# Performance work log

Hardware: AMD Instinct MI355X
Metric: run time of the kernel (lower is better)

Reference implementation:

```python
import jax, jax.numpy as jnp
import numpy as np

B, T_IN, T_OUT, F, H = 1024, 168, 24, 8, 256


def _lstm_step(x, h, c, Wih, Whh, bih, bhh):
    # x: [B, in], h/c: [B, H]; PyTorch gate order i, f, g, o
    g = x @ Wih.T + h @ Whh.T + bih + bhh
    i, f, gg, o = jnp.split(g, 4, axis=-1)
    i = jax.nn.sigmoid(i)
    f = jax.nn.sigmoid(f)
    gg = jnp.tanh(gg)
    o = jax.nn.sigmoid(o)
    c2 = f * c + i * gg
    h2 = o * jnp.tanh(c2)
    return h2, c2


def _run_lstm(xs, Wih, Whh, bih, bhh):
    # xs: [T, B, in] -> (ys [T,B,H], h_T, c_T)
    Bs = xs.shape[1]
    h0 = jnp.zeros((Bs, H), xs.dtype)
    c0 = jnp.zeros((Bs, H), xs.dtype)
    def step(carry, x):
        h, c = carry
        h2, c2 = _lstm_step(x, h, c, Wih, Whh, bih, bhh)
        return (h2, c2), h2
    (hT, cT), ys = jax.lax.scan(step, (h0, c0), xs)
    return ys, hT, cT


def _forward(x, enc_Wih0, enc_Whh0, enc_bih0, enc_bhh0,
             enc_Wih1, enc_Whh1, enc_bih1, enc_bhh1,
             dec_Wih, dec_Whh, dec_bih, dec_bhh,
             fc1_W, fc1_b, attn_in_W, attn_in_b,
             attn_out_W, attn_out_b, fc2_W, fc2_b):
    scale = 1.0 / jnp.sqrt(jnp.asarray(H, x.dtype))

    # ---- encoder: 2-layer LSTM ----
    xs = jnp.transpose(x, (1, 0, 2))  # [T, B, F]
    ys0, h0, c0 = _run_lstm(xs, enc_Wih0, enc_Whh0, enc_bih0, enc_bhh0)
    _, h1, c1 = _run_lstm(ys0, enc_Wih1, enc_Whh1, enc_bih1, enc_bhh1)
    h_mean = (h0 + h1) * 0.5  # mean over layers, [B, H]
    c_mean = (c0 + c1) * 0.5

    # per-decoder initial state (same mean state for every decoder at t=0)
    h_state = jnp.tile(h_mean[None], (F, 1, 1))  # [F, B, H]
    c_state = jnp.tile(c_mean[None], (F, 1, 1))
    dec_in = x[:, -1, :]  # [B, F]

    def dec_one(xi, h, c, Wih, Whh, bih, bhh, f1W, f1b, inW, inb, oW, ob, f2W, f2b):
        # xi: [B, 1], single-feature single-step LSTM decode
        h2, c2 = _lstm_step(xi, h, c, Wih, Whh, bih, bhh)  # [B, H]
        a = jax.nn.leaky_relu(h2 @ f1W.T + f1b, 0.01)  # q = k = v
        qkv = a @ inW.T + inb  # [B, 3H]
        q, k, v = jnp.split(qkv, 3, axis=-1)
        # NB: faithful to the original bug: MultiheadAttention sees the batch
        # dim as the sequence dim, so attention is over the B examples.
        attn = jax.nn.softmax((q @ k.T) * scale, axis=-1)  # [B, B]
        ao = (attn @ v) @ oW.T + ob  # [B, H]
        out = jax.nn.leaky_relu(ao @ f2W.T + f2b, 0.01)  # [B, 1]
        return out[:, 0], h2, c2

    dec_all = jax.vmap(dec_one)  # over the F decoders

    def outer(carry, _):
        h, c, din = carry
        xi = din.T[:, :, None]  # [F, B, 1]
        out, h2, c2 = dec_all(xi, h, c, dec_Wih, dec_Whh, dec_bih, dec_bhh,
                              fc1_W, fc1_b, attn_in_W, attn_in_b,
                              attn_out_W, attn_out_b, fc2_W, fc2_b)
        return (h2, c2, out.T), out  # out: [F, B]

    _, outs = jax.lax.scan(outer, (h_state, c_state, dec_in), None, length=T_OUT)
    return jnp.transpose(outs, (2, 0, 1))  # [B, T_OUT, F]


def setup_inputs() -> dict:
    key = jax.random.key(0)
    ks = jax.random.split(key, 22)
    p = lambda k, shape: jax.random.normal(k, shape, dtype=jnp.float32) * 0.05
    return {
        "x": jax.random.normal(ks[0], (B, T_IN, F), dtype=jnp.float32),
        "enc_Wih0": p(ks[1], (4 * H, F)),
        "enc_Whh0": p(ks[2], (4 * H, H)),
        "enc_bih0": p(ks[3], (4 * H,)),
        "enc_bhh0": p(ks[4], (4 * H,)),
        "enc_Wih1": p(ks[5], (4 * H, H)),
        "enc_Whh1": p(ks[6], (4 * H, H)),
        "enc_bih1": p(ks[7], (4 * H,)),
        "enc_bhh1": p(ks[8], (4 * H,)),
        "dec_Wih": p(ks[9], (F, 4 * H, 1)),
        "dec_Whh": p(ks[10], (F, 4 * H, H)),
        "dec_bih": p(ks[11], (F, 4 * H)),
        "dec_bhh": p(ks[12], (F, 4 * H)),
        "fc1_W": p(ks[13], (F, H, H)),
        "fc1_b": p(ks[14], (F, H)),
        "attn_in_W": p(ks[15], (F, 3 * H, H)),
        "attn_in_b": p(ks[16], (F, 3 * H)),
        "attn_out_W": p(ks[17], (F, H, H)),
        "attn_out_b": p(ks[18], (F, H)),
        "fc2_W": p(ks[19], (F, 1, H)),
        "fc2_b": p(ks[20], (F, 1)),
    }


def reference(x, enc_Wih0, enc_Whh0, enc_bih0, enc_bhh0,
              enc_Wih1, enc_Whh1, enc_bih1, enc_bhh1,
              dec_Wih, dec_Whh, dec_bih, dec_bhh,
              fc1_W, fc1_b, attn_in_W, attn_in_b,
              attn_out_W, attn_out_b, fc2_W, fc2_b):
    return _forward(x, enc_Wih0, enc_Whh0, enc_bih0, enc_bhh0,
                    enc_Wih1, enc_Whh1, enc_bih1, enc_bhh1,
                    dec_Wih, dec_Whh, dec_bih, dec_bhh,
                    fc1_W, fc1_b, attn_in_W, attn_in_b,
                    attn_out_W, attn_out_b, fc2_W, fc2_b)
```

## Files before the change

### kernel.cpp

```cpp
#include <hip/hip_runtime.h>
#include <math.h>

#define H 256
#define H4 1024
#define Bsz 1024
#define TIN 168
#define TOUT 24
#define Fh 8
#define XROW (TIN*Fh)
#define BH ((size_t)Bsz * H)
#define SL32 ((size_t)Bsz * 32)

typedef __attribute__((ext_vector_type(8))) short bf16x8;
typedef __attribute__((ext_vector_type(4))) float f32x4;

__device__ __forceinline__ ushort f2bf(float f) {
    union { float f; unsigned u; } v; v.f = f;
    unsigned r = v.u + 0x7fff + ((v.u >> 16) & 1);
    return (ushort)(r >> 16);
}
__device__ __forceinline__ float bf2f(ushort u) {
    union { unsigned u; float f; } v; v.u = ((unsigned)u) << 16;
    return v.f;
}
__device__ __forceinline__ float sigmf(float x) {
    return __fdividef(1.0f, 1.0f + __expf(-x));
}
__device__ __forceinline__ float tanhf_(float x) {
    const float e = __expf(-2.0f * fabsf(x));
    const float t = __fdividef(1.0f - e, 1.0f + e);
    return copysignf(t, x);
}

__device__ __forceinline__ void load_coh4(const ushort* p0, const ushort* p1,
                                          const ushort* p2, const ushort* p3,
                                          f32x4& a, f32x4& b, f32x4& c, f32x4& d)
{
    asm volatile(
        "global_load_dwordx4 %0, %4, off sc0 sc1\n\t"
        "global_load_dwordx4 %1, %5, off sc0 sc1\n\t"
        "global_load_dwordx4 %2, %6, off sc0 sc1\n\t"
        "global_load_dwordx4 %3, %7, off sc0 sc1\n\t"
        "s_waitcnt vmcnt(0)"
        : "=&v"(a), "=&v"(b), "=&v"(c), "=&v"(d)
        : "v"(p0), "v"(p1), "v"(p2), "v"(p3)
        : "memory");
}
__device__ __forceinline__ void load_coh8(const ushort* p0, const ushort* p1,
                                          const ushort* p2, const ushort* p3,
                                          const ushort* p4, const ushort* p5,
                                          const ushort* p6, const ushort* p7,
                                          f32x4& a, f32x4& b, f32x4& c, f32x4& d,
                                          f32x4& e, f32x4& f, f32x4& g, f32x4& h)
{
    asm volatile(
        "global_load_dwordx4 %0, %8, off sc0 sc1\n\t"
        "global_load_dwordx4 %1, %9, off sc0 sc1\n\t"
        "global_load_dwordx4 %2, %10, off sc0 sc1\n\t"
        "global_load_dwordx4 %3, %11, off sc0 sc1\n\t"
        "global_load_dwordx4 %4, %12, off sc0 sc1\n\t"
        "global_load_dwordx4 %5, %13, off sc0 sc1\n\t"
        "global_load_dwordx4 %6, %14, off sc0 sc1\n\t"
        "global_load_dwordx4 %7, %15, off sc0 sc1\n\t"
        "s_waitcnt vmcnt(0)"
        : "=&v"(a), "=&v"(b), "=&v"(c), "=&v"(d),
          "=&v"(e), "=&v"(f), "=&v"(g), "=&v"(h)
        : "v"(p0), "v"(p1), "v"(p2), "v"(p3), "v"(p4), "v"(p5), "v"(p6), "v"(p7)
        : "memory");
}
__device__ __forceinline__ void load_coh4f(const float* p0, const float* p1,
                                           const float* p2, const float* p3,
                                           float& a, float& b, float& c, float& d)
{
    asm volatile(
        "global_load_dword %0, %4, off sc0 sc1\n\t"
        "global_load_dword %1, %5, off sc0 sc1\n\t"
        "global_load_dword %2, %6, off sc0 sc1\n\t"
        "global_load_dword %3, %7, off sc0 sc1\n\t"
        "s_waitcnt vmcnt(0)"
        : "=&v"(a), "=&v"(b), "=&v"(c), "=&v"(d)
        : "v"(p0), "v"(p1), "v"(p2), "v"(p3)
        : "memory");
}
__device__ __forceinline__ void store_coh8B(ushort* p, uint2 v) {
    asm volatile("global_store_dwordx2 %0, %1, off sc0 sc1"
                 :: "v"(p), "v"(v) : "memory");
}
__device__ __forceinline__ void store_coh16B(float* p, f32x4 v) {
    asm volatile("global_store_dwordx4 %0, %1, off sc0 sc1"
                 :: "v"(p), "v"(v) : "memory");
}

__device__ __forceinline__ void load_l2_8(const ushort* p0, const ushort* p1,
                                          const ushort* p2, const ushort* p3,
                                          const ushort* p4, const ushort* p5,
                                          const ushort* p6, const ushort* p7,
                                          f32x4& a, f32x4& b, f32x4& c, f32x4& d,
                                          f32x4& e, f32x4& f, f32x4& g, f32x4& h)
{
    asm volatile(
        "global_load_dwordx4 %0, %8, off sc0\n\t"
        "global_load_dwordx4 %1, %9, off sc0\n\t"
        "global_load_dwordx4 %2, %10, off sc0\n\t"
        "global_load_dwordx4 %3, %11, off sc0\n\t"
        "global_load_dwordx4 %4, %12, off sc0\n\t"
        "global_load_dwordx4 %5, %13, off sc0\n\t"
        "global_load_dwordx4 %6, %14, off sc0\n\t"
        "global_load_dwordx4 %7, %15, off sc0\n\t"
        "s_waitcnt vmcnt(0)"
        : "=&v"(a), "=&v"(b), "=&v"(c), "=&v"(d),
          "=&v"(e), "=&v"(f), "=&v"(g), "=&v"(h)
        : "v"(p0), "v"(p1), "v"(p2), "v"(p3), "v"(p4), "v"(p5), "v"(p6), "v"(p7)
        : "memory");
}
__device__ __forceinline__ void load_l2_f4(const float* p, f32x4& v) {
    asm volatile(
        "global_load_dwordx4 %0, %1, off sc0\n\t"
        "s_waitcnt vmcnt(0)"
        : "=&v"(v) : "v"(p) : "memory");
}

__device__ __forceinline__ void gbar(unsigned* cnt, unsigned target) {
    asm volatile("s_waitcnt vmcnt(0)" ::: "memory");
    __syncthreads();
    if (threadIdx.x == 0) {
        __hip_atomic_fetch_add(cnt, 1u, __ATOMIC_RELAXED, __HIP_MEMORY_SCOPE_AGENT);
        int sp = 0;
        while (__hip_atomic_fetch_add(cnt, 0u, __ATOMIC_RELAXED,
                                      __HIP_MEMORY_SCOPE_AGENT) < target) {
            __builtin_amdgcn_s_sleep(2);
            if (++sp > 20000) break;
        }
    }
    __syncthreads();
    asm volatile("" ::: "memory");
}

__global__ __launch_bounds__(256)
void cast_f32_bf16(const float* __restrict__ in, ushort* __restrict__ out, int n) {
    int i = blockIdx.x * 256 + threadIdx.x;
    const int stride = gridDim.x * 256;
    for (; i < n; i += stride) out[i] = f2bf(in[i]);
// ... 27 lines not shown
    u[f * 256 + tid] = su;
    if (tid == 0) {
        float dd = 0.f, cc = 0.f;
        for (int n = 0; n < 256; ++n) dd += wsh[n] * inb[f * 768 + 512 + n];
        for (int i = 0; i < 256; ++i) cc += ob[f * 256 + i] * f2W[f * 256 + i];
        dconst[f] = dd;
        ccv[f] = cc + f2b[f];
    }
}

struct MP {
    const float *x, *ebih0, *ebhh0, *ebih1, *ebhh1;
    const ushort *Whh0, *Wih0p, *Wih1, *Whh1;
    ushort *h0A, *h0B, *h1A, *h1B, *hm;
    float *cm;
    const ushort *dWhh, *f1Wb, *inWb;
    const float *dWih, *dbih, *dbhh, *f1b, *inb, *u, *dconst, *ccv;
    ushort *kb0, *kb1;
    float *vw0, *vw1, *out;
    unsigned *bar;
};

__global__ __launch_bounds__(256, 1)
void mega2(MP P)
{
    __shared__ ushort SA[32][264];
    __shared__ ushort SB[32][264];
    __shared__ ushort SC[32][264];
    __shared__ float pre[4][32][36];
    __shared__ ushort xL[32][32];
    __shared__ ushort h2s[32][264];
    __shared__ ushort as2[32][264];
    __shared__ ushort qs[32][264];
    __shared__ float tri[4][2][16][3];
    __shared__ float dinL[32];

    const int bid = blockIdx.x;
    const int tid = threadIdx.x;
    const int l = tid & 63, w = tid >> 6;
    const int lr = l & 15, lq = l >> 4, lk = lq * 8;

    {
        const int grp = bid >> 3, wgi = bid & 7;
        const int rowbase = grp * 32;
        const int ub = wgi * 32;
        unsigned* cnt = P.bar + grp * 32;
        const int g = w;
        const int sS = tid >> 5, sR = tid & 31;

        for (int e = tid; e < 32 * 32; e += 256) (&xL[0][0])[e] = 0;

        const int crow = tid >> 3;
        const int cu = (tid & 7) * 4;
        float c0v[4] = {0,0,0,0}, c1v[4] = {0,0,0,0};
        float h0v[4] = {0,0,0,0}, h1v[4] = {0,0,0,0};

        float b0s[2], b1s[2];
#pragma unroll
        for (int n = 0; n < 2; ++n) {
            const int j = ub + n * 16 + lr;
            b0s[n] = P.ebih0[g * H + j] + P.ebhh0[g * H + j];
            b1s[n] = P.ebih1[g * H + j] + P.ebhh1[g * H + j];
        }
        unsigned bph = 0;
        __syncthreads();

        for (int t = 0; t < TIN; ++t) {
            const int p = t & 1;
            const ushort* h0r = p ? P.h0B : P.h0A;
            ushort*       h0w = p ? P.h0A : P.h0B;
            const ushort* h1r = p ? P.h1B : P.h1A;
            ushort*       h1w = p ? P.h1A : P.h1B;

            {
                const ushort* s0 = h0r + sS * SL32 + (size_t)(rowbase + sR) * 32;
                f32x4 v0, v1, v2, v3;
                load_coh4(s0, s0 + 8, s0 + 16, s0 + 24, v0, v1, v2, v3);
                *(f32x4*)&SA[sR][sS * 32 + 0]  = v0;
                *(f32x4*)&SA[sR][sS * 32 + 8]  = v1;
                *(f32x4*)&SA[sR][sS * 32 + 16] = v2;
                *(f32x4*)&SA[sR][sS * 32 + 24] = v3;
                xL[tid >> 3][tid & 7] =
                    f2bf(P.x[(size_t)(rowbase + (tid >> 3)) * XROW + t * Fh + (tid & 7)]);
            }
            __syncthreads();
            {
                bf16x8 am[2][8], ax[2];
#pragma unroll
                for (int m = 0; m < 2; ++m) {
#pragma unroll
                    for (int k = 0; k < 8; ++k)
                        am[m][k] = *(const bf16x8*)&SA[m * 16 + lr][k * 32 + lk];
                    ax[m] = *(const bf16x8*)&xL[m * 16 + lr][lk];
                }
                f32x4 acc[2][2] = {};
#pragma unroll
                for (int n = 0; n < 2; ++n) {
                    const ushort* wp = P.Whh0 + (size_t)(g * H + ub + n * 16 + lr) * H + lk;
#pragma unroll
                    for (int k = 0; k < 8; ++k) {
                        const bf16x8 b8 = *(const bf16x8*)(wp + k * 32);
                        acc[0][n] = __builtin_amdgcn_mfma_f32_16x16x32_bf16(am[0][k], b8, acc[0][n], 0, 0, 0);
                        acc[1][n] = __builtin_amdgcn_mfma_f32_16x16x32_bf16(am[1][k], b8, acc[1][n], 0, 0, 0);
                    }
                    const bf16x8 bx = *(const bf16x8*)(P.Wih0p + (size_t)(g * H + ub + n * 16 + lr) * 32 + lk);
                    acc[0][n] = __builtin_amdgcn_mfma_f32_16x16x32_bf16(ax[0], bx, acc[0][n], 0, 0, 0);
                    acc[1][n] = __builtin_amdgcn_mfma_f32_16x16x32_bf16(ax[1], bx, acc[1][n], 0, 0, 0);
                }
#pragma unroll
                for (int m = 0; m < 2; ++m)
#pragma unroll
                    for (int n = 0; n < 2; ++n)
#pragma unroll
                        for (int r = 0; r < 4; ++r)
                            pre[g][m * 16 + lq * 4 + r][n * 16 + lr] = acc[m][n][r] + b0s[n];
            }
            __syncthreads();
            {
                const f32x4 pi = *(const f32x4*)&pre[0][crow][cu];
                const f32x4 pf = *(const f32x4*)&pre[1][crow][cu];
                const f32x4 pg = *(const f32x4*)&pre[2][crow][cu];
                const f32x4 po = *(const f32x4*)&pre[3][crow][cu];
#pragma unroll
                for (int j = 0; j < 4; ++j) {
                    const float ig = sigmf(pi[j]);
                    const float fg = sigmf(pf[j]);
                    const float gg = tanhf_(pg[j]);
                    const float og = sigmf(po[j]);
                    c0v[j] = fg * c0v[j] + ig * gg;
                    h0v[j] = og * tanhf_(c0v[j]);
                }
                uint2 hp;
                hp.x = (unsigned)f2bf(h0v[0]) | ((unsigned)f2bf(h0v[1]) << 16);
                hp.y = (unsigned)f2bf(h0v[2]) | ((unsigned)f2bf(h0v[3]) << 16);
                store_coh8B(h0w + wgi * SL32 + (size_t)(rowbase + crow) * 32 + cu, hp);
            }
            gbar(cnt, ++bph * 8u);
            {
                const ushort* s0 = h0w + sS * SL32 + (size_t)(rowbase + sR) * 32;
                const ushort* s1 = h1r + sS * SL32 + (size_t)(rowbase + sR) * 32;
                f32x4 a0, a1, a2, a3, b0, b1, b2, b3;
                load_coh8(s0, s0 + 8, s0 + 16, s0 + 24,
                          s1, s1 + 8, s1 + 16, s1 + 24,
                          a0, a1, a2, a3, b0, b1, b2, b3);
                *(f32x4*)&SB[sR][sS * 32 + 0]  = a0;
                *(f32x4*)&SB[sR][sS * 32 + 8]  = a1;
                *(f32x4*)&SB[sR][sS * 32 + 16] = a2;
                *(f32x4*)&SB[sR][sS * 32 + 24] = a3;
                *(f32x4*)&SC[sR][sS * 32 + 0]  = b0;
                *(f32x4*)&SC[sR][sS * 32 + 8]  = b1;
                *(f32x4*)&SC[sR][sS * 32 + 16] = b2;
                *(f32x4*)&SC[sR][sS * 32 + 24] = b3;
            }
            __syncthreads();
            {
                bf16x8 an[2][8], ah[2][8];
#pragma unroll
                for (int m = 0; m < 2; ++m)
#pragma unroll
                    for (int k = 0; k < 8; ++k) {
                        an[m][k] = *(const bf16x8*)&SB[m * 16 + lr][k * 32 + lk];
                        ah[m][k] = *(const bf16x8*)&SC[m * 16 + lr][k * 32 + lk];
                    }
                f32x4 acc[2][2] = {};
#pragma unroll
                for (int n = 0; n < 2; ++n) {
                    const ushort* w1 = P.Wih1 + (size_t)(g * H + ub + n * 16 + lr) * H + lk;
                    const ushort* w2 = P.Whh1 + (size_t)(g * H + ub + n * 16 + lr) * H + lk;
#pragma unroll
                    for (int k = 0; k < 8; ++k) {
                        const bf16x8 b1 = *(const bf16x8*)(w1 + k * 32);
                        acc[0][n] = __builtin_amdgcn_mfma_f32_16x16x32_bf16(an[0][k], b1, acc[0][n], 0, 0, 0);
                        acc[1][n] = __builtin_amdgcn_mfma_f32_16x16x32_bf16(an[1][k], b1, acc[1][n], 0, 0, 0);
                        const bf16x8 b2 = *(const bf16x8*)(w2 + k * 32);
                        acc[0][n] = __builtin_amdgcn_mfma_f32_16x16x32_bf16(ah[0][k], b2, acc[0][n], 0, 0, 0);
                        acc[1][n] = __builtin_amdgcn_mfma_f32_16x16x32_bf16(ah[1][k], b2, acc[1][n], 0, 0, 0);
                    }
                }
#pragma unroll
                for (int m = 0; m < 2; ++m)
#pragma unroll
                    for (int n = 0; n < 2; ++n)
#pragma unroll
                        for (int r = 0; r < 4; ++r)
                            pre[g][m * 16 + lq * 4 + r][n * 16 + lr] = acc[m][n][r] + b1s[n];
            }
            __syncthreads();
            {
                const f32x4 pi = *(const f32x4*)&pre[0][crow][cu];
                const f32x4 pf = *(const f32x4*)&pre[1][crow][cu];
                const f32x4 pg = *(const f32x4*)&pre[2][crow][cu];
                const f32x4 po = *(const f32x4*)&pre[3][crow][cu];
#pragma unroll
                for (int j = 0; j < 4; ++j) {
                    const float ig = sigmf(pi[j]);
                    const float fg = sigmf(pf[j]);
                    const float gg = tanhf_(pg[j]);
                    const float og = sigmf(po[j]);
                    c1v[j] = fg * c1v[j] + ig * gg;
                    h1v[j] = og * tanhf_(c1v[j]);
                }
                uint2 hp;
                hp.x = (unsigned)f2bf(h1v[0]) | ((unsigned)f2bf(h1v[1]) << 16);
                hp.y = (unsigned)f2bf(h1v[2]) | ((unsigned)f2bf(h1v[3]) << 16);
                store_coh8B(h1w + wgi * SL32 + (size_t)(rowbase + crow) * 32 + cu, hp);
            }
            gbar(cnt, ++bph * 8u);
        }
        {
            uint2 hp;
            hp.x = (unsigned)f2bf(0.5f * (h0v[0] + h1v[0]))
                 | ((unsigned)f2bf(0.5f * (h0v[1] + h1v[1])) << 16);
            hp.y = (unsigned)f2bf(0.5f * (h0v[2] + h1v[2]))
                 | ((unsigned)f2bf(0.5f * (h0v[3] + h1v[3])) << 16);
            store_coh8B(P.hm + (size_t)(rowbase + crow) * 256 + ub + cu, hp);
            f32x4 cv;
#pragma unroll
            for (int j = 0; j < 4; ++j) cv[j] = 0.5f * (c0v[j] + c1v[j]);
            store_coh16B(P.cm + (size_t)(rowbase + crow) * 256 + ub + cu, cv);
        }
    }
    gbar(P.bar + 2048, 256u);

    {
        const int f = bid & 7, mb = bid >> 3;
        const int m0 = mb * 32;

#pragma unroll
        for (int it = 0; it < 4; ++it) {
            const int idx = tid + it * 256;
            const int r = idx >> 5, c16 = (idx & 31) * 8;
            f32x4 v0, v1, v2, v3;
            const ushort* pbase = P.hm + (size_t)(m0 + r) * 256 + c16;
            asm volatile("global_load_dwordx4 %0, %1, off sc0 sc1\n\ts_waitcnt vmcnt(0)"
                         : "=&v"(v0) : "v"(pbase) : "memory");
            *(f32x4*)&h2s[r][c16] = v0;
            (void)v1; (void)v2; (void)v3;
        }
        float cd[2][4][4];
#pragma unroll
        for (int m = 0; m < 2; ++m)
#pragma unroll
            for (int jt = 0; jt < 4; ++jt) {
                const float* pc = P.cm + (size_t)(m0 + m * 16 + lq * 4) * 256
                                + (w * 64 + jt * 16 + lr);
                load_coh4f(pc, pc + 256, pc + 512, pc + 768,
                           cd[m][jt][0], cd[m][jt][1], cd[m][jt][2], cd[m][jt][3]);
            }
        float bsum[4][4], wxr[4][4];
#pragma unroll
        for (int jt = 0; jt < 4; ++jt)
#pragma unroll
            for (int g = 0; g < 4; ++g) {
                const int j = w * 64 + jt * 16 + lr;
                bsum[jt][g] = P.dbih[f * H4 + g * H + j] + P.dbhh[f * H4 + g * H + j];
                wxr[jt][g] = P.dWih[f * H4 + g * H + j];
            }
        __syncthreads();

        unsigned* fcnt = P.bar + 1024 + f * 32;
// ... 114 lines not shown
#pragma unroll 1
                for (int rr = 0; rr < 8; ++rr) {
                    const int mloc = w * 8 + rr;
                    const ushort4 a4 = *(const ushort4*)&as2[mloc][l * 4];
                    float s = bf2f(a4.x) * u4.x + bf2f(a4.y) * u4.y
                            + bf2f(a4.z) * u4.z + bf2f(a4.w) * u4.w;
#pragma unroll
                    for (int d = 1; d < 64; d <<= 1) s += __shfl_xor(s, d);
                    if (l == 0) vwcur[f * Bsz + m0 + mloc] = s + P.dconst[f];
                }
            }
            gbar(fcnt, (unsigned)(t + 1) * 32u);
            {
                bf16x8 qf[2][8];
#pragma unroll
                for (int m = 0; m < 2; ++m)
#pragma unroll
                    for (int k = 0; k < 8; ++k)
                        qf[m][k] = *(const bf16x8*)&qs[m * 16 + lr][k * 32 + lk];
                float mM0 = -1e30f, lS0 = 0.f, oS0 = 0.f;
                float mM1 = -1e30f, lS1 = 0.f, oS1 = 0.f;
                const int kb0r = w * 256;
#pragma unroll 1
                for (int kf = 0; kf < 16; ++kf) {
                    const int kb = kb0r + kf * 16;
                    const ushort* base = kcur + ((size_t)f * Bsz + kb + lr) * H + lk;
                    f32x4 kr0, kr1, kr2, kr3, kr4, kr5, kr6, kr7;
                    load_l2_8(base, base + 32, base + 64, base + 96,
                              base + 128, base + 160, base + 192, base + 224,
                              kr0, kr1, kr2, kr3, kr4, kr5, kr6, kr7);
                    f32x4 acc0 = {}, acc1 = {};
                    {
                        const bf16x8 kk0 = *(bf16x8*)&kr0, kk1 = *(bf16x8*)&kr1,
                                     kk2 = *(bf16x8*)&kr2, kk3 = *(bf16x8*)&kr3,
                                     kk4 = *(bf16x8*)&kr4, kk5 = *(bf16x8*)&kr5,
                                     kk6 = *(bf16x8*)&kr6, kk7 = *(bf16x8*)&kr7;
                        acc0 = __builtin_amdgcn_mfma_f32_16x16x32_bf16(kk0, qf[0][0], acc0, 0, 0, 0);
                        acc1 = __builtin_amdgcn_mfma_f32_16x16x32_bf16(kk0, qf[1][0], acc1, 0, 0, 0);
                        acc0 = __builtin_amdgcn_mfma_f32_16x16x32_bf16(kk1, qf[0][1], acc0, 0, 0, 0);
                        acc1 = __builtin_amdgcn_mfma_f32_16x16x32_bf16(kk1, qf[1][1], acc1, 0, 0, 0);
                        acc0 = __builtin_amdgcn_mfma_f32_16x16x32_bf16(kk2, qf[0][2], acc0, 0, 0, 0);
                        acc1 = __builtin_amdgcn_mfma_f32_16x16x32_bf16(kk2, qf[1][2], acc1, 0, 0, 0);
                        acc0 = __builtin_amdgcn_mfma_f32_16x16x32_bf16(kk3, qf[0][3], acc0, 0, 0, 0);
                        acc1 = __builtin_amdgcn_mfma_f32_16x16x32_bf16(kk3, qf[1][3], acc1, 0, 0, 0);
                        acc0 = __builtin_amdgcn_mfma_f32_16x16x32_bf16(kk4, qf[0][4], acc0, 0, 0, 0);
                        acc1 = __builtin_amdgcn_mfma_f32_16x16x32_bf16(kk4, qf[1][4], acc1, 0, 0, 0);
                        acc0 = __builtin_amdgcn_mfma_f32_16x16x32_bf16(kk5, qf[0][5], acc0, 0, 0, 0);
                        acc1 = __builtin_amdgcn_mfma_f32_16x16x32_bf16(kk5, qf[1][5], acc1, 0, 0, 0);
                        acc0 = __builtin_amdgcn_mfma_f32_16x16x32_bf16(kk6, qf[0][6], acc0, 0, 0, 0);
                        acc1 = __builtin_amdgcn_mfma_f32_16x16x32_bf16(kk6, qf[1][6], acc1, 0, 0, 0);
                        acc0 = __builtin_amdgcn_mfma_f32_16x16x32_bf16(kk7, qf[0][7], acc0, 0, 0, 0);
                        acc1 = __builtin_amdgcn_mfma_f32_16x16x32_bf16(kk7, qf[1][7], acc1, 0, 0, 0);
                    }
                    f32x4 v4w;
                    load_l2_f4(vwcur + f * Bsz + kb + lq * 4, v4w);
                    {
                        const float mx = fmaxf(fmaxf(acc0[0], acc0[1]), fmaxf(acc0[2], acc0[3]));
                        const float mn = fmaxf(mM0, mx);
                        const float sc = __expf(mM0 - mn);
                        const float e0 = __expf(acc0[0] - mn), e1 = __expf(acc0[1] - mn);
                        const float e2 = __expf(acc0[2] - mn), e3 = __expf(acc0[3] - mn);
                        lS0 = lS0 * sc + (e0 + e1 + e2 + e3);
                        oS0 = oS0 * sc + (e0 * v4w[0] + e1 * v4w[1] + e2 * v4w[2] + e3 * v4w[3]);
                        mM0 = mn;
                    }
                    {
                        const float mx = fmaxf(fmaxf(acc1[0], acc1[1]), fmaxf(acc1[2], acc1[3]));
                        const float mn = fmaxf(mM1, mx);
                        const float sc = __expf(mM1 - mn);
                        const float e0 = __expf(acc1[0] - mn), e1 = __expf(acc1[1] - mn);
                        const float e2 = __expf(acc1[2] - mn), e3 = __expf(acc1[3] - mn);
                        lS1 = lS1 * sc + (e0 + e1 + e2 + e3);
                        oS1 = oS1 * sc + (e0 * v4w[0] + e1 * v4w[1] + e2 * v4w[2] + e3 * v4w[3]);
                        mM1 = mn;
                    }
                }
#pragma unroll
                for (int d = 16; d < 64; d <<= 1) {
                    {
                        const float m2 = __shfl_xor(mM0, d), l2 = __shfl_xor(lS0, d), o2 = __shfl_xor(oS0, d);
                        const float mn = fmaxf(mM0, m2);
                        const float sa = __expf(mM0 - mn), sb = __expf(m2 - mn);
                        lS0 = lS0 * sa + l2 * sb; oS0 = oS0 * sa + o2 * sb; mM0 = mn;
                    }
                    {
                        const float m2 = __shfl_xor(mM1, d), l2 = __shfl_xor(lS1, d), o2 = __shfl_xor(oS1, d);
                        const float mn = fmaxf(mM1, m2);
                        const float sa = __expf(mM1 - mn), sb = __expf(m2 - mn);
                        lS1 = lS1 * sa + l2 * sb; oS1 = oS1 * sa + o2 * sb; mM1 = mn;
                    }
                }
                if (l < 16) {
                    tri[w][0][l][0] = mM0; tri[w][0][l][1] = lS0; tri[w][0][l][2] = oS0;
                    tri[w][1][l][0] = mM1; tri[w][1][l][1] = lS1; tri[w][1][l][2] = oS1;
                }
                __syncthreads();
                if (tid < 32) {
// ... 51 lines not shown
    ushort* h1A = (ushort*)alloc(BH * 2);
    ushort* h0B = (ushort*)alloc(BH * 2);
    ushort* h1B = (ushort*)alloc(BH * 2);
    ushort* hm  = (ushort*)alloc(BH * 2);
    float*  cm  = (float*)alloc(BH * 4);
    ushort* kb0 = (ushort*)alloc(8 * BH * 2);
    ushort* kb1 = (ushort*)alloc(8 * BH * 2);
    float*  vw0 = (float*)alloc((size_t)Fh * Bsz * 4);
    float*  vw1 = (float*)alloc((size_t)Fh * Bsz * 4);
    float*  ubuf = (float*)alloc((size_t)Fh * H * 4);
    float*  dbuf = (float*)alloc(Fh * 4);
    float*  ccb  = (float*)alloc(Fh * 4);
    unsigned* bar = (unsigned*)alloc(3072 * 4);
    ushort* wWhh0 = (ushort*)alloc((size_t)H4 * H * 2);
    ushort* wWih0p= (ushort*)alloc((size_t)H4 * 32 * 2);
    ushort* wWih1 = (ushort*)alloc((size_t)H4 * H * 2);
    ushort* wWhh1 = (ushort*)alloc((size_t)H4 * H * 2);
    ushort* wdWhh = (ushort*)alloc((size_t)8 * H4 * H * 2);
    ushort* wf1W  = (ushort*)alloc((size_t)8 * H * H * 2);
    ushort* winW  = (ushort*)alloc((size_t)8 * 768 * H * 2);

    const dim3 blk(256);

    hipMemsetAsync(d_ws, 0, BH * 2 * 2, stream);
    hipMemsetAsync(bar, 0, 3072 * 4, stream);

    cast_f32_bf16<<<dim3(512), blk, 0, stream>>>(eWhh0, wWhh0, H4 * H);
    cast_f32_bf16<<<dim3(512), blk, 0, stream>>>(eWih1, wWih1, H4 * H);
    cast_f32_bf16<<<dim3(512), blk, 0, stream>>>(eWhh1, wWhh1, H4 * H);
    cast_pad_wih0<<<dim3(128), blk, 0, stream>>>(eWih0, wWih0p);
    cast_f32_bf16<<<dim3(1024), blk, 0, stream>>>(dWhh, wdWhh, 8 * H4 * H);
    cast_f32_bf16<<<dim3(512), blk, 0, stream>>>(f1W, wf1W, 8 * H * H);
    cast_f32_bf16<<<dim3(1024), blk, 0, stream>>>(inW, winW, 8 * 768 * H);
    precompute_kernel<<<dim3(8), blk, 0, stream>>>(oW, ob, f2W, f2b, inW, inb,
                                                   ubuf, dbuf, ccb);

    MP P;
    P.x = x; P.ebih0 = ebih0; P.ebhh0 = ebhh0; P.ebih1 = ebih1; P.ebhh1 = ebhh1;
    P.Whh0 = wWhh0; P.Wih0p = wWih0p; P.Wih1 = wWih1; P.Whh1 = wWhh1;
    P.h0A = h0A; P.h0B = h0B; P.h1A = h1A; P.h1B = h1B;
    P.hm = hm; P.cm = cm;
    P.dWhh = wdWhh; P.f1Wb = wf1W; P.inWb = winW;
    P.dWih = dWih; P.dbih = dbih; P.dbhh = dbhh; P.f1b = f1b; P.inb = inb;
    P.u = ubuf; P.dconst = dbuf; P.ccv = ccb;
    P.kb0 = kb0; P.kb1 = kb1; P.vw0 = vw0; P.vw1 = vw1;
    P.out = (float*)d_out; P.bar = bar;

    mega2<<<dim3(256), blk, 0, stream>>>(P);

    (void)in_sizes; (void)n_in; (void)out_size; (void)ws_size;
}
```

Measured before the change: 3.568 ms.

## Wavefront-pipeline encoder layers to halve grid barriers; batch attention key loads

The two-layer encoder loop is skewed so that layer 1 at step t-1 and layer 0 at step t run in the same iteration. Each step now needs one grid-wide barrier and one coherent load phase instead of two, and one shared h0 tile feeds both the layer-0 recurrent matmul and the layer-1 input matmul. The decoder attention loop is also unrolled by two: K and V loads for two 16-row chunks are issued together with immediate offsets before the waitcnt. The trade-off is one extra loop iteration, separate pre-activation buffers per layer, more registers, and a wider zero memset so both layers' h buffers start cleared.

Result: faster. 3.237 ms (-9.3%).

```diff
diff --git a/kernel.cpp b/kernel.cpp
--- a/kernel.cpp
+++ b/kernel.cpp
@@ -32,20 +32,6 @@
     return copysignf(t, x);
 }
 
-__device__ __forceinline__ void load_coh4(const ushort* p0, const ushort* p1,
-                                          const ushort* p2, const ushort* p3,
-                                          f32x4& a, f32x4& b, f32x4& c, f32x4& d)
-{
-    asm volatile(
-        "global_load_dwordx4 %0, %4, off sc0 sc1\n\t"
-        "global_load_dwordx4 %1, %5, off sc0 sc1\n\t"
-        "global_load_dwordx4 %2, %6, off sc0 sc1\n\t"
-        "global_load_dwordx4 %3, %7, off sc0 sc1\n\t"
-        "s_waitcnt vmcnt(0)"
-        : "=&v"(a), "=&v"(b), "=&v"(c), "=&v"(d)
-        : "v"(p0), "v"(p1), "v"(p2), "v"(p3)
-        : "memory");
-}
 __device__ __forceinline__ void load_coh8(const ushort* p0, const ushort* p1,
                                           const ushort* p2, const ushort* p3,
                                           const ushort* p4, const ushort* p5,
@@ -82,6 +68,10 @@
         : "v"(p0), "v"(p1), "v"(p2), "v"(p3)
         : "memory");
 }
+__device__ __forceinline__ void load_coh16Bx(const ushort* p, f32x4& v) {
+    asm volatile("global_load_dwordx4 %0, %1, off sc0 sc1\n\ts_waitcnt vmcnt(0)"
+                 : "=&v"(v) : "v"(p) : "memory");
+}
 __device__ __forceinline__ void store_coh8B(ushort* p, uint2 v) {
     asm volatile("global_store_dwordx2 %0, %1, off sc0 sc1"
                  :: "v"(p), "v"(v) : "memory");
@@ -89,35 +79,6 @@
 __device__ __forceinline__ void store_coh16B(float* p, f32x4 v) {
     asm volatile("global_store_dwordx4 %0, %1, off sc0 sc1"
                  :: "v"(p), "v"(v) : "memory");
-}
-
-__device__ __forceinline__ void load_l2_8(const ushort* p0, const ushort* p1,
-                                          const ushort* p2, const ushort* p3,
-                                          const ushort* p4, const ushort* p5,
-                                          const ushort* p6, const ushort* p7,
-                                          f32x4& a, f32x4& b, f32x4& c, f32x4& d,
-                                          f32x4& e, f32x4& f, f32x4& g, f32x4& h)
-{
-    asm volatile(
-        "global_load_dwordx4 %0, %8, off sc0\n\t"
-        "global_load_dwordx4 %1, %9, off sc0\n\t"
-        "global_load_dwordx4 %2, %10, off sc0\n\t"
-        "global_load_dwordx4 %3, %11, off sc0\n\t"
-        "global_load_dwordx4 %4, %12, off sc0\n\t"
-        "global_load_dwordx4 %5, %13, off sc0\n\t"
-        "global_load_dwordx4 %6, %14, off sc0\n\t"
-        "global_load_dwordx4 %7, %15, off sc0\n\t"
-        "s_waitcnt vmcnt(0)"
-        : "=&v"(a), "=&v"(b), "=&v"(c), "=&v"(d),
-          "=&v"(e), "=&v"(f), "=&v"(g), "=&v"(h)
-        : "v"(p0), "v"(p1), "v"(p2), "v"(p3), "v"(p4), "v"(p5), "v"(p6), "v"(p7)
-        : "memory");
-}
-__device__ __forceinline__ void load_l2_f4(const float* p, f32x4& v) {
-    asm volatile(
-        "global_load_dwordx4 %0, %1, off sc0\n\t"
-        "s_waitcnt vmcnt(0)"
-        : "=&v"(v) : "v"(p) : "memory");
 }
 
 __device__ __forceinline__ void gbar(unsigned* cnt, unsigned target) {
@@ -191,12 +152,12 @@
 };
 
 __global__ __launch_bounds__(256, 1)
-void mega2(MP P)
+void mega3(MP P)
 {
     __shared__ ushort SA[32][264];
-    __shared__ ushort SB[32][264];
     __shared__ ushort SC[32][264];
-    __shared__ float pre[4][32][36];
+    __shared__ float pre0[4][32][36];
+    __shared__ float pre1[4][32][36];
     __shared__ ushort xL[32][32];
     __shared__ ushort h2s[32][264];
     __shared__ ushort as2[32][264];
@@ -234,34 +195,45 @@
         unsigned bph = 0;
         __syncthreads();
 
-        for (int t = 0; t < TIN; ++t) {
-            const int p = t & 1;
-            const ushort* h0r = p ? P.h0B : P.h0A;
-            ushort*       h0w = p ? P.h0A : P.h0B;
-            const ushort* h1r = p ? P.h1B : P.h1A;
-            ushort*       h1w = p ? P.h1A : P.h1B;
+        for (int i = 0; i <= TIN; ++i) {
+            ushort*       h0wb = (i & 1) ? P.h0B : P.h0A;
+            const ushort* h0rb = (i & 1) ? P.h0A : P.h0B;
+            ushort*       h1wb = (i & 1) ? P.h1A : P.h1B;
+            const ushort* h1rb = (i & 1) ? P.h1B : P.h1A;
 
             {
-                const ushort* s0 = h0r + sS * SL32 + (size_t)(rowbase + sR) * 32;
-                f32x4 v0, v1, v2, v3;
-                load_coh4(s0, s0 + 8, s0 + 16, s0 + 24, v0, v1, v2, v3);
-                *(f32x4*)&SA[sR][sS * 32 + 0]  = v0;
-                *(f32x4*)&SA[sR][sS * 32 + 8]  = v1;
-                *(f32x4*)&SA[sR][sS * 32 + 16] = v2;
-                *(f32x4*)&SA[sR][sS * 32 + 24] = v3;
-                xL[tid >> 3][tid & 7] =
-                    f2bf(P.x[(size_t)(rowbase + (tid >> 3)) * XROW + t * Fh + (tid & 7)]);
+                const ushort* s0 = h0rb + sS * SL32 + (size_t)(rowbase + sR) * 32;
+                const ushort* s1 = h1rb + sS * SL32 + (size_t)(rowbase + sR) * 32;
+                f32x4 a0, a1, a2, a3, b0, b1, b2, b3;
+                load_coh8(s0, s0 + 8, s0 + 16, s0 + 24,
+                          s1, s1 + 8, s1 + 16, s1 + 24,
+                          a0, a1, a2, a3, b0, b1, b2, b3);
+                *(f32x4*)&SA[sR][sS * 32 + 0]  = a0;
+                *(f32x4*)&SA[sR][sS * 32 + 8]  = a1;
+                *(f32x4*)&SA[sR][sS * 32 + 16] = a2;
+                *(f32x4*)&SA[sR][sS * 32 + 24] = a3;
+                *(f32x4*)&SC[sR][sS * 32 + 0]  = b0;
+                *(f32x4*)&SC[sR][sS * 32 + 8]  = b1;
+                *(f32x4*)&SC[sR][sS * 32 + 16] = b2;
+                *(f32x4*)&SC[sR][sS * 32 + 24] = b3;
+                if (i < TIN)
+                    xL[tid >> 3][tid & 7] =
+                        f2bf(P.x[(size_t)(rowbase + (tid >> 3)) * XROW + i * Fh + (tid & 7)]);
             }
             __syncthreads();
-            {
-                bf16x8 am[2][8], ax[2];
-#pragma unroll
-                for (int m = 0; m < 2; ++m) {
-#pragma unroll
-                    for (int k = 0; k < 8; ++k)
-                        am[m][k] = *(const bf16x8*)&SA[m * 16 + lr][k * 32 + lk];
-                    ax[m] = *(const bf16x8*)&xL[m * 16 + lr][lk];
-                }
+
+            bf16x8 aS[2][8], aC[2][8], ax[2];
+#pragma unroll
+            for (int m = 0; m < 2; ++m) {
+#pragma unroll
+                for (int k = 0; k < 8; ++k) {
+                    aS[m][k] = *(const bf16x8*)&SA[m * 16 + lr][k * 32 + lk];
+                    aC[m][k] = *(const bf16x8*)&SC[m * 16 + lr][k * 32 + lk];
+                }
+                ax[m] = *(const bf16x8*)&xL[m * 16 + lr][lk];
+            }
+
+            if (i < TIN) {
                 f32x4 acc[2][2] = {};
 #pragma unroll
                 for (int n = 0; n < 2; ++n) {
@@ -269,8 +241,8 @@
 #pragma unroll
                     for (int k = 0; k < 8; ++k) {
                         const bf16x8 b8 = *(const bf16x8*)(wp + k * 32);
-                        acc[0][n] = __builtin_amdgcn_mfma_f32_16x16x32_bf16(am[0][k], b8, acc[0][n], 0, 0, 0);
-                        acc[1][n] = __builtin_amdgcn_mfma_f32_16x16x32_bf16(am[1][k], b8, acc[1][n], 0, 0, 0);
+                        acc[0][n] = __builtin_amdgcn_mfma_f32_16x16x32_bf16(aS[0][k], b8, acc[0][n], 0, 0, 0);
+                        acc[1][n] = __builtin_amdgcn_mfma_f32_16x16x32_bf16(aS[1][k], b8, acc[1][n], 0, 0, 0);
                     }
                     const bf16x8 bx = *(const bf16x8*)(P.Wih0p + (size_t)(g * H + ub + n * 16 + lr) * 32 + lk);
                     acc[0][n] = __builtin_amdgcn_mfma_f32_16x16x32_bf16(ax[0], bx, acc[0][n], 0, 0, 0);
@@ -282,14 +254,39 @@
                     for (int n = 0; n < 2; ++n)
 #pragma unroll
                         for (int r = 0; r < 4; ++r)
-                            pre[g][m * 16 + lq * 4 + r][n * 16 + lr] = acc[m][n][r] + b0s[n];
+                            pre0[g][m * 16 + lq * 4 + r][n * 16 + lr] = acc[m][n][r] + b0s[n];
+            }
+            if (i >= 1) {
+                f32x4 acc[2][2] = {};
+#pragma unroll
+                for (int n = 0; n < 2; ++n) {
+                    const ushort* w1 = P.Wih1 + (size_t)(g * H + ub + n * 16 + lr) * H + lk;
+                    const ushort* w2 = P.Whh1 + (size_t)(g * H + ub + n * 16 + lr) * H + lk;
+#pragma unroll
+                    for (int k = 0; k < 8; ++k) {
+                        const bf16x8 b1 = *(const bf16x8*)(w1 + k * 32);
+                        acc[0][n] = __builtin_amdgcn_mfma_f32_16x16x32_bf16(aS[0][k], b1, acc[0][n], 0, 0, 0);
+                        acc[1][n] = __builtin_amdgcn_mfma_f32_16x16x32_bf16(aS[1][k], b1, acc[1][n], 0, 0, 0);
+                        const bf16x8 b2 = *(const bf16x8*)(w2 + k * 32);
+                        acc[0][n] = __builtin_amdgcn_mfma_f32_16x16x32_bf16(aC[0][k], b2, acc[0][n], 0, 0, 0);
+                        acc[1][n] = __builtin_amdgcn_mfma_f32_16x16x32_bf16(aC[1][k], b2, acc[1][n], 0, 0, 0);
+                    }
+                }
+#pragma unroll
+                for (int m = 0; m < 2; ++m)
+#pragma unroll
+                    for (int n = 0; n < 2; ++n)
+#pragma unroll
+                        for (int r = 0; r < 4; ++r)
+                            pre1[g][m * 16 + lq * 4 + r][n * 16 + lr] = acc[m][n][r] + b1s[n];
             }
             __syncthreads();
-            {
-                const f32x4 pi = *(const f32x4*)&pre[0][crow][cu];
-                const f32x4 pf = *(const f32x4*)&pre[1][crow][cu];
-                const f32x4 pg = *(const f32x4*)&pre[2][crow][cu];
-                const f32x4 po = *(const f32x4*)&pre[3][crow][cu];
+
+            if (i < TIN) {
+                const f32x4 pi = *(const f32x4*)&pre0[0][crow][cu];
+                const f32x4 pf = *(const f32x4*)&pre0[1][crow][cu];
+                const f32x4 pg = *(const f32x4*)&pre0[2][crow][cu];
+                const f32x4 po = *(const f32x4*)&pre0[3][crow][cu];
 #pragma unroll
                 for (int j = 0; j < 4; ++j) {
                     const float ig = sigmf(pi[j]);
@@ -302,64 +299,13 @@
                 uint2 hp;
                 hp.x = (unsigned)f2bf(h0v[0]) | ((unsigned)f2bf(h0v[1]) << 16);
                 hp.y = (unsigned)f2bf(h0v[2]) | ((unsigned)f2bf(h0v[3]) << 16);
-                store_coh8B(h0w + wgi * SL32 + (size_t)(rowbase + crow) * 32 + cu, hp);
-            }
-            gbar(cnt, ++bph * 8u);
-            {
-                const ushort* s0 = h0w + sS * SL32 + (size_t)(rowbase + sR) * 32;
-                const ushort* s1 = h1r + sS * SL32 + (size_t)(rowbase + sR) * 32;
-                f32x4 a0, a1, a2, a3, b0, b1, b2, b3;
-                load_coh8(s0, s0 + 8, s0 + 16, s0 + 24,
-                          s1, s1 + 8, s1 + 16, s1 + 24,
-                          a0, a1, a2, a3, b0, b1, b2, b3);
-                *(f32x4*)&SB[sR][sS * 32 + 0]  = a0;
-                *(f32x4*)&SB[sR][sS * 32 + 8]  = a1;
-                *(f32x4*)&SB[sR][sS * 32 + 16] = a2;
-                *(f32x4*)&SB[sR][sS * 32 + 24] = a3;
-                *(f32x4*)&SC[sR][sS * 32 + 0]  = b0;
-                *(f32x4*)&SC[sR][sS * 32 + 8]  = b1;
-                *(f32x4*)&SC[sR][sS * 32 + 16] = b2;
-                *(f32x4*)&SC[sR][sS * 32 + 24] = b3;
-            }
-            __syncthreads();
-            {
-                bf16x8 an[2][8], ah[2][8];
-#pragma unroll
-                for (int m = 0; m < 2; ++m)
-#pragma unroll
-                    for (int k = 0; k < 8; ++k) {
-                        an[m][k] = *(const bf16x8*)&SB[m * 16 + lr][k * 32 + lk];
-                        ah[m][k] = *(const bf16x8*)&SC[m * 16 + lr][k * 32 + lk];
-                    }
-                f32x4 acc[2][2] = {};
-#pragma unroll
-                for (int n = 0; n < 2; ++n) {
-                    const ushort* w1 = P.Wih1 + (size_t)(g * H + ub + n * 16 + lr) * H + lk;
-                    const ushort* w2 = P.Whh1 + (size_t)(g * H + ub + n * 16 + lr) * H + lk;
-#pragma unroll
-                    for (int k = 0; k < 8; ++k) {
-                        const bf16x8 b1 = *(const bf16x8*)(w1 + k * 32);
-                        acc[0][n] = __builtin_amdgcn_mfma_f32_16x16x32_bf16(an[0][k], b1, acc[0][n], 0, 0, 0);
-                        acc[1][n] = __builtin_amdgcn_mfma_f32_16x16x32_bf16(an[1][k], b1, acc[1][n], 0, 0, 0);
-                        const bf16x8 b2 = *(const bf16x8*)(w2 + k * 32);
-                        acc[0][n] = __builtin_amdgcn_mfma_f32_16x16x32_bf16(ah[0][k], b2, acc[0][n], 0, 0, 0);
-                        acc[1][n] = __builtin_amdgcn_mfma_f32_16x16x32_bf16(ah[1][k], b2, acc[1][n], 0, 0, 0);
-                    }
-                }
-#pragma unroll
-                for (int m = 0; m < 2; ++m)
-#pragma unroll
-                    for (int n = 0; n < 2; ++n)
-#pragma unroll
-                        for (int r = 0; r < 4; ++r)
-                            pre[g][m * 16 + lq * 4 + r][n * 16 + lr] = acc[m][n][r] + b1s[n];
-            }
-            __syncthreads();
-            {
-                const f32x4 pi = *(const f32x4*)&pre[0][crow][cu];
-                const f32x4 pf = *(const f32x4*)&pre[1][crow][cu];
-                const f32x4 pg = *(const f32x4*)&pre[2][crow][cu];
-                const f32x4 po = *(const f32x4*)&pre[3][crow][cu];
+                store_coh8B(h0wb + wgi * SL32 + (size_t)(rowbase + crow) * 32 + cu, hp);
+            }
+            if (i >= 1) {
+                const f32x4 pi = *(const f32x4*)&pre1[0][crow][cu];
+                const f32x4 pf = *(const f32x4*)&pre1[1][crow][cu];
+                const f32x4 pg = *(const f32x4*)&pre1[2][crow][cu];
+                const f32x4 po = *(const f32x4*)&pre1[3][crow][cu];
 #pragma unroll
                 for (int j = 0; j < 4; ++j) {
                     const float ig = sigmf(pi[j]);
@@ -372,7 +318,7 @@
                 uint2 hp;
                 hp.x = (unsigned)f2bf(h1v[0]) | ((unsigned)f2bf(h1v[1]) << 16);
                 hp.y = (unsigned)f2bf(h1v[2]) | ((unsigned)f2bf(h1v[3]) << 16);
-                store_coh8B(h1w + wgi * SL32 + (size_t)(rowbase + crow) * 32 + cu, hp);
+                store_coh8B(h1wb + wgi * SL32 + (size_t)(rowbase + crow) * 32 + cu, hp);
             }
             gbar(cnt, ++bph * 8u);
         }
@@ -399,12 +345,9 @@
         for (int it = 0; it < 4; ++it) {
             const int idx = tid + it * 256;
             const int r = idx >> 5, c16 = (idx & 31) * 8;
-            f32x4 v0, v1, v2, v3;
-            const ushort* pbase = P.hm + (size_t)(m0 + r) * 256 + c16;
-            asm volatile("global_load_dwordx4 %0, %1, off sc0 sc1\n\ts_waitcnt vmcnt(0)"
-                         : "=&v"(v0) : "v"(pbase) : "memory");
+            f32x4 v0;
+            load_coh16Bx(P.hm + (size_t)(m0 + r) * 256 + c16, v0);
             *(f32x4*)&h2s[r][c16] = v0;
-            (void)v1; (void)v2; (void)v3;
         }
         float cd[2][4][4];
 #pragma unroll
@@ -565,57 +508,128 @@
                 float mM1 = -1e30f, lS1 = 0.f, oS1 = 0.f;
                 const int kb0r = w * 256;
 #pragma unroll 1
-                for (int kf = 0; kf < 16; ++kf) {
-                    const int kb = kb0r + kf * 16;
-                    const ushort* base = kcur + ((size_t)f * Bsz + kb + lr) * H + lk;
-                    f32x4 kr0, kr1, kr2, kr3, kr4, kr5, kr6, kr7;
-                    load_l2_8(base, base + 32, base + 64, base + 96,
-                              base + 128, base + 160, base + 192, base + 224,
-                              kr0, kr1, kr2, kr3, kr4, kr5, kr6, kr7);
-                    f32x4 acc0 = {}, acc1 = {};
+                for (int kf = 0; kf < 16; kf += 2) {
+                    const int kbA = kb0r + kf * 16;
+                    const ushort* baseA = kcur + ((size_t)f * Bsz + kbA + lr) * H + lk;
+                    const ushort* baseB = baseA + 16 * H;
+                    const float* pvA = vwcur + f * Bsz + kbA + lq * 4;
+                    const float* pvB = pvA + 16;
+                    f32x4 A0, A1, A2, A3, A4, A5, A6, A7;
+                    f32x4 B0, B1, B2, B3, B4, B5, B6, B7;
+                    f32x4 vA, vB;
+                    asm volatile(
+                        "global_load_dwordx4 %0, %18, off sc0\n\t"
+                        "global_load_dwordx4 %1, %18, off offset:64 sc0\n\t"
+                        "global_load_dwordx4 %2, %18, off offset:128 sc0\n\t"
+                        "global_load_dwordx4 %3, %18, off offset:192 sc0\n\t"
+                        "global_load_dwordx4 %4, %18, off offset:256 sc0\n\t"
+                        "global_load_dwordx4 %5, %18, off offset:320 sc0\n\t"
+                        "global_load_dwordx4 %6, %18, off offset:384 sc0\n\t"
+                        "global_load_dwordx4 %7, %18, off offset:448 sc0\n\t"
+                        "global_load_dwordx4 %8, %19, off sc0\n\t"
+                        "global_load_dwordx4 %9, %19, off offset:64 sc0\n\t"
+                        "global_load_dwordx4 %10, %19, off offset:128 sc0\n\t"
+                        "global_load_dwordx4 %11, %19, off offset:192 sc0\n\t"
+                        "global_load_dwordx4 %12, %19, off offset:256 sc0\n\t"
+                        "global_load_dwordx4 %13, %19, off offset:320 sc0\n\t"
+                        "global_load_dwordx4 %14, %19, off offset:384 sc0\n\t"
+                        "global_load_dwordx4 %15, %19, off offset:448 sc0\n\t"
+                        "global_load_dwordx4 %16, %20, off sc0\n\t"
+                        "global_load_dwordx4 %17, %21, off sc0\n\t"
+                        "s_waitcnt vmcnt(0)"
+                        : "=&v"(A0), "=&v"(A1), "=&v"(A2), "=&v"(A3),
+                          "=&v"(A4), "=&v"(A5), "=&v"(A6), "=&v"(A7),
+                          "=&v"(B0), "=&v"(B1), "=&v"(B2), "=&v"(B3),
+                          "=&v"(B4), "=&v"(B5), "=&v"(B6), "=&v"(B7),
+                          "=&v"(vA), "=&v"(vB)
+                        : "v"(baseA), "v"(baseB), "v"(pvA), "v"(pvB)
+                        : "memory");
+                    __builtin_amdgcn_sched_barrier(0);
                     {
-                        const bf16x8 kk0 = *(bf16x8*)&kr0, kk1 = *(bf16x8*)&kr1,
-                                     kk2 = *(bf16x8*)&kr2, kk3 = *(bf16x8*)&kr3,
-                                     kk4 = *(bf16x8*)&kr4, kk5 = *(bf16x8*)&kr5,
-                                     kk6 = *(bf16x8*)&kr6, kk7 = *(bf16x8*)&kr7;
-                        acc0 = __builtin_amdgcn_mfma_f32_16x16x32_bf16(kk0, qf[0][0], acc0, 0, 0, 0);
-                        acc1 = __builtin_amdgcn_mfma_f32_16x16x32_bf16(kk0, qf[1][0], acc1, 0, 0, 0);
-                        acc0 = __builtin_amdgcn_mfma_f32_16x16x32_bf16(kk1, qf[0][1], acc0, 0, 0, 0);
-                        acc1 = __builtin_amdgcn_mfma_f32_16x16x32_bf16(kk1, qf[1][1], acc1, 0, 0, 0);
-                        acc0 = __builtin_amdgcn_mfma_f32_16x16x32_bf16(kk2, qf[0][2], acc0, 0, 0, 0);
-                        acc1 = __builtin_amdgcn_mfma_f32_16x16x32_bf16(kk2, qf[1][2], acc1, 0, 0, 0);
-                        acc0 = __builtin_amdgcn_mfma_f32_16x16x32_bf16(kk3, qf[0][3], acc0, 0, 0, 0);
-                        acc1 = __builtin_amdgcn_mfma_f32_16x16x32_bf16(kk3, qf[1][3], acc1, 0, 0, 0);
-                        acc0 = __builtin_amdgcn_mfma_f32_16x16x32_bf16(kk4, qf[0][4], acc0, 0, 0, 0);
-                        acc1 = __builtin_amdgcn_mfma_f32_16x16x32_bf16(kk4, qf[1][4], acc1, 0, 0, 0);
-                        acc0 = __builtin_amdgcn_mfma_f32_16x16x32_bf16(kk5, qf[0][5], acc0, 0, 0, 0);
-                        acc1 = __builtin_amdgcn_mfma_f32_16x16x32_bf16(kk5, qf[1][5], acc1, 0, 0, 0);
-                        acc0 = __builtin_amdgcn_mfma_f32_16x16x32_bf16(kk6, qf[0][6], acc0, 0, 0, 0);
-                        acc1 = __builtin_amdgcn_mfma_f32_16x16x32_bf16(kk6, qf[1][6], acc1, 0, 0, 0);
-                        acc0 = __builtin_amdgcn_mfma_f32_16x16x32_bf16(kk7, qf[0][7], acc0, 0, 0, 0);
-                        acc1 = __builtin_amdgcn_mfma_f32_16x16x32_bf16(kk7, qf[1][7], acc1, 0, 0, 0);
-                    }
-                    f32x4 v4w;
-                    load_l2_f4(vwcur + f * Bsz + kb + lq * 4, v4w);
+                        f32x4 acc0 = {}, acc1 = {};
+                        const bf16x8 k0 = *(bf16x8*)&A0, k1 = *(bf16x8*)&A1,
+                                     k2 = *(bf16x8*)&A2, k3 = *(bf16x8*)&A3,
+                                     k4 = *(bf16x8*)&A4, k5 = *(bf16x8*)&A5,
+                                     k6 = *(bf16x8*)&A6, k7 = *(bf16x8*)&A7;
+                        acc0 = __builtin_amdgcn_mfma_f32_16x16x32_bf16(k0, qf[0][0], acc0, 0, 0, 0);
+                        acc1 = __builtin_amdgcn_mfma_f32_16x16x32_bf16(k0, qf[1][0], acc1, 0, 0, 0);
+                        acc0 = __builtin_amdgcn_mfma_f32_16x16x32_bf16(k1, qf[0][1], acc0, 0, 0, 0);
+                        acc1 = __builtin_amdgcn_mfma_f32_16x16x32_bf16(k1, qf[1][1], acc1, 0, 0, 0);
+                        acc0 = __builtin_amdgcn_mfma_f32_16x16x32_bf16(k2, qf[0][2], acc0, 0, 0, 0);
+                        acc1 = __builtin_amdgcn_mfma_f32_16x16x32_bf16(k2, qf[1][2], acc1, 0, 0, 0);
+                        acc0 = __builtin_amdgcn_mfma_f32_16x16x32_bf16(k3, qf[0][3], acc0, 0, 0, 0);
+                        acc1 = __builtin_amdgcn_mfma_f32_16x16x32_bf16(k3, qf[1][3], acc1, 0, 0, 0);
+                        acc0 = __builtin_amdgcn_mfma_f32_16x16x32_bf16(k4, qf[0][4], acc0, 0, 0, 0);
+                        acc1 = __builtin_amdgcn_mfma_f32_16x16x32_bf16(k4, qf[1][4], acc1, 0, 0, 0);
+                        acc0 = __builtin_amdgcn_mfma_f32_16x16x32_bf16(k5, qf[0][5], acc0, 0, 0, 0);
+                        acc1 = __builtin_amdgcn_mfma_f32_16x16x32_bf16(k5, qf[1][5], acc1, 0, 0, 0);
+                        acc0 = __builtin_amdgcn_mfma_f32_16x16x32_bf16(k6, qf[0][6], acc0, 0, 0, 0);
+                        acc1 = __builtin_amdgcn_mfma_f32_16x16x32_bf16(k6, qf[1][6], acc1, 0, 0, 0);
+                        acc0 = __builtin_amdgcn_mfma_f32_16x16x32_bf16(k7, qf[0][7], acc0, 0, 0, 0);
+                        acc1 = __builtin_amdgcn_mfma_f32_16x16x32_bf16(k7, qf[1][7], acc1, 0, 0, 0);
+                        {
+                            const float mx = fmaxf(fmaxf(acc0[0], acc0[1]), fmaxf(acc0[2], acc0[3]));
+                            const float mn = fmaxf(mM0, mx);
+                            const float sc = __expf(mM0 - mn);
+                            const float e0 = __expf(acc0[0] - mn), e1 = __expf(acc0[1] - mn);
+                            const float e2 = __expf(acc0[2] - mn), e3 = __expf(acc0[3] - mn);
+                            lS0 = lS0 * sc + (e0 + e1 + e2 + e3);
+                            oS0 = oS0 * sc + (e0 * vA[0] + e1 * vA[1] + e2 * vA[2] + e3 * vA[3]);
+                            mM0 = mn;
+                        }
+                        {
+                            const float mx = fmaxf(fmaxf(acc1[0], acc1[1]), fmaxf(acc1[2], acc1[3]));
+                            const float mn = fmaxf(mM1, mx);
+                            const float sc = __expf(mM1 - mn);
+                            const float e0 = __expf(acc1[0] - mn), e1 = __expf(acc1[1] - mn);
+                            const float e2 = __expf(acc1[2] - mn), e3 = __expf(acc1[3] - mn);
+                            lS1 = lS1 * sc + (e0 + e1 + e2 + e3);
+                            oS1 = oS1 * sc + (e0 * vA[0] + e1 * vA[1] + e2 * vA[2] + e3 * vA[3]);
+                            mM1 = mn;
+                        }
+                    }
                     {
-                        const float mx = fmaxf(fmaxf(acc0[0], acc0[1]), fmaxf(acc0[2], acc0[3]));
-                        const float mn = fmaxf(mM0, mx);
-                        const float sc = __expf(mM0 - mn);
-                        const float e0 = __expf(acc0[0] - mn), e1 = __expf(acc0[1] - mn);
-                        const float e2 = __expf(acc0[2] - mn), e3 = __expf(acc0[3] - mn);
-                        lS0 = lS0 * sc + (e0 + e1 + e2 + e3);
-                        oS0 = oS0 * sc + (e0 * v4w[0] + e1 * v4w[1] + e2 * v4w[2] + e3 * v4w[3]);
-                        mM0 = mn;
-                    }
-                    {
-                        const float mx = fmaxf(fmaxf(acc1[0], acc1[1]), fmaxf(acc1[2], acc1[3]));
-                        const float mn = fmaxf(mM1, mx);
-                        const float sc = __expf(mM1 - mn);
-                        const float e0 = __expf(acc1[0] - mn), e1 = __expf(acc1[1] - mn);
-                        const float e2 = __expf(acc1[2] - mn), e3 = __expf(acc1[3] - mn);
-                        lS1 = lS1 * sc + (e0 + e1 + e2 + e3);
-                        oS1 = oS1 * sc + (e0 * v4w[0] + e1 * v4w[1] + e2 * v4w[2] + e3 * v4w[3]);
-                        mM1 = mn;
+                        f32x4 acc0 = {}, acc1 = {};
+                        const bf16x8 k0 = *(bf16x8*)&B0, k1 = *(bf16x8*)&B1,
+                                     k2 = *(bf16x8*)&B2, k3 = *(bf16x8*)&B3,
+                                     k4 = *(bf16x8*)&B4, k5 = *(bf16x8*)&B5,
+                                     k6 = *(bf16x8*)&B6, k7 = *(bf16x8*)&B7;
+                        acc0 = __builtin_amdgcn_mfma_f32_16x16x32_bf16(k0, qf[0][0], acc0, 0, 0, 0);
+                        acc1 = __builtin_amdgcn_mfma_f32_16x16x32_bf16(k0, qf[1][0], acc1, 0, 0, 0);
+                        acc0 = __builtin_amdgcn_mfma_f32_16x16x32_bf16(k1, qf[0][1], acc0, 0, 0, 0);
+                        acc1 = __builtin_amdgcn_mfma_f32_16x16x32_bf16(k1, qf[1][1], acc1, 0, 0, 0);
+                        acc0 = __builtin_amdgcn_mfma_f32_16x16x32_bf16(k2, qf[0][2], acc0, 0, 0, 0);
+                        acc1 = __builtin_amdgcn_mfma_f32_16x16x32_bf16(k2, qf[1][2], acc1, 0, 0, 0);
+                        acc0 = __builtin_amdgcn_mfma_f32_16x16x32_bf16(k3, qf[0][3], acc0, 0, 0, 0);
+                        acc1 = __builtin_amdgcn_mfma_f32_16x16x32_bf16(k3, qf[1][3], acc1, 0, 0, 0);
+                        acc0 = __builtin_amdgcn_mfma_f32_16x16x32_bf16(k4, qf[0][4], acc0, 0, 0, 0);
+                        acc1 = __builtin_amdgcn_mfma_f32_16x16x32_bf16(k4, qf[1][4], acc1, 0, 0, 0);
+                        acc0 = __builtin_amdgcn_mfma_f32_16x16x32_bf16(k5, qf[0][5], acc0, 0, 0, 0);
+                        acc1 = __builtin_amdgcn_mfma_f32_16x16x32_bf16(k5, qf[1][5], acc1, 0, 0, 0);
+                        acc0 = __builtin_amdgcn_mfma_f32_16x16x32_bf16(k6, qf[0][6], acc0, 0, 0, 0);
+                        acc1 = __builtin_amdgcn_mfma_f32_16x16x32_bf16(k6, qf[1][6], acc1, 0, 0, 0);
+                        acc0 = __builtin_amdgcn_mfma_f32_16x16x32_bf16(k7, qf[0][7], acc0, 0, 0, 0);
+                        acc1 = __builtin_amdgcn_mfma_f32_16x16x32_bf16(k7, qf[1][7], acc1, 0, 0, 0);
+                        {
+                            const float mx = fmaxf(fmaxf(acc0[0], acc0[1]), fmaxf(acc0[2], acc0[3]));
+                            const float mn = fmaxf(mM0, mx);
+                            const float sc = __expf(mM0 - mn);
+                            const float e0 = __expf(acc0[0] - mn), e1 = __expf(acc0[1] - mn);
+                            const float e2 = __expf(acc0[2] - mn), e3 = __expf(acc0[3] - mn);
+                            lS0 = lS0 * sc + (e0 + e1 + e2 + e3);
+                            oS0 = oS0 * sc + (e0 * vB[0] + e1 * vB[1] + e2 * vB[2] + e3 * vB[3]);
+                            mM0 = mn;
+                        }
+                        {
+                            const float mx = fmaxf(fmaxf(acc1[0], acc1[1]), fmaxf(acc1[2], acc1[3]));
+                            const float mn = fmaxf(mM1, mx);
+                            const float sc = __expf(mM1 - mn);
+                            const float e0 = __expf(acc1[0] - mn), e1 = __expf(acc1[1] - mn);
+                            const float e2 = __expf(acc1[2] - mn), e3 = __expf(acc1[3] - mn);
+                            lS1 = lS1 * sc + (e0 + e1 + e2 + e3);
+                            oS1 = oS1 * sc + (e0 * vB[0] + e1 * vB[1] + e2 * vB[2] + e3 * vB[3]);
+                            mM1 = mn;
+                        }
                     }
                 }
 #pragma unroll
@@ -713,7 +727,7 @@
 
     const dim3 blk(256);
 
-    hipMemsetAsync(d_ws, 0, BH * 2 * 2, stream);
+    hipMemsetAsync(d_ws, 0, BH * 2 * 4, stream);
     hipMemsetAsync(bar, 0, 3072 * 4, stream);
 
     cast_f32_bf16<<<dim3(512), blk, 0, stream>>>(eWhh0, wWhh0, H4 * H);
@@ -737,7 +751,7 @@
     P.kb0 = kb0; P.kb1 = kb1; P.vw0 = vw0; P.vw1 = vw1;
     P.out = (float*)d_out; P.bar = bar;
 
-    mega2<<<dim3(256), blk, 0, stream>>>(P);
+    mega3<<<dim3(256), blk, 0, stream>>>(P);
 
     (void)in_sizes; (void)n_in; (void)out_size; (void)ws_size;
 }
```
